# Optimization experiments

Measured on AMD Instinct MI355X. Metric: run time of the kernel, lower is better.

Reference implementation:

```python
import jax, jax.numpy as jnp
import numpy as np
import math

D_MODEL = 1024
H = 16
D_K = D_MODEL // H
D_FF = 4096
NEG = -1e9


def layer_norm(x, alpha, bias):
    # Faithful to source: mean over last dim, UNBIASED std (torch.std default),
    # eps defined in source but never used in forward.
    mean = jnp.mean(x, axis=-1, keepdims=True)
    std = jnp.std(x, axis=-1, ddof=1, keepdims=True)
    return (x - mean) / std * alpha + bias


def mha(x, mask, w_q, w_k, w_v, w_o):
    B, S, D = x.shape
    q = (x @ w_q.T).reshape(B, S, H, D_K)
    k = (x @ w_k.T).reshape(B, S, H, D_K)
    v = (x @ w_v.T).reshape(B, S, H, D_K)
    scores = jnp.einsum('bqhd,bkhd->bhqk', q, k) / math.sqrt(D_K)
    scores = jnp.where(mask, NEG, scores)
    attn = jax.nn.softmax(scores, axis=-1)
    out = jnp.einsum('bhqk,bkhd->bqhd', attn, v).reshape(B, S, D)
    return out @ w_o.T


def setup_inputs() -> dict:
    key = jax.random.key(0)
    ks = jax.random.split(key, 16)
    B, S = 4, 2048
    s = 0.02
    return {
        'x': jax.random.normal(ks[0], (B, S, D_MODEL), jnp.float32),
        'w_q': jax.random.normal(ks[1], (D_MODEL, D_MODEL), jnp.float32) * s,
        'w_k': jax.random.normal(ks[2], (D_MODEL, D_MODEL), jnp.float32) * s,
        'w_v': jax.random.normal(ks[3], (D_MODEL, D_MODEL), jnp.float32) * s,
        'w_o': jax.random.normal(ks[4], (D_MODEL, D_MODEL), jnp.float32) * s,
        'l1_w': jax.random.normal(ks[5], (D_FF, D_MODEL), jnp.float32) * s,
        'l1_b': jnp.zeros((D_FF,), jnp.float32),
        'l2_w': jax.random.normal(ks[6], (D_MODEL, D_FF), jnp.float32) * s,
        'l2_b': jnp.zeros((D_MODEL,), jnp.float32),
        'norm1_a': jnp.ones((D_MODEL,), jnp.float32),
        'norm1_b': jnp.zeros((D_MODEL,), jnp.float32),
        'norm2_a': jnp.ones((D_MODEL,), jnp.float32),
        'norm2_b': jnp.zeros((D_MODEL,), jnp.float32),
        'normf_a': jnp.ones((D_MODEL,), jnp.float32),
        'normf_b': jnp.zeros((D_MODEL,), jnp.float32),
        'mask': jax.random.randint(ks[7], (B, 1, 1, S), 0, 2) == 1,
    }


def reference(x, w_q, w_k, w_v, w_o, l1_w, l1_b, l2_w, l2_b,
              norm1_a, norm1_b, norm2_a, norm2_b, normf_a, normf_b, mask):
    # residual 1: pre-norm self-attention (dropout is identity at eval)
    x = x + mha(layer_norm(x, norm1_a, norm1_b), mask, w_q, w_k, w_v, w_o)
    # residual 2: pre-norm FFN
    h = layer_norm(x, norm2_a, norm2_b)
    ff = jax.nn.relu(h @ l1_w.T + l1_b) @ l2_w.T + l2_b
    x = x + ff
    return layer_norm(x, normf_a, normf_b)
```

## Files before the change

kernel.cpp:

```cpp
#include <hip/hip_runtime.h>
#include <hip/hip_bf16.h>


typedef __bf16 bf16x8 __attribute__((ext_vector_type(8)));
typedef float f32x4 __attribute__((ext_vector_type(4)));
typedef unsigned short u16x8 __attribute__((ext_vector_type(8)));
using bf16 = __hip_bfloat16;

__device__ __forceinline__ f32x4 mfma16(bf16x8 a, bf16x8 b, f32x4 c) {
  return __builtin_amdgcn_mfma_f32_16x16x32_bf16(a, b, c, 0, 0, 0);
}

__device__ __forceinline__ int swz(int row, int blk) {
  return row * 64 + ((blk ^ (row & 7)) << 3);
}

__device__ __forceinline__ void stage_tile64(unsigned short* lds,
                                             const bf16* g, int ld, int rows) {
  const int lane = threadIdx.x & 63, wid = threadIdx.x >> 6;
  const int r8 = lane >> 3, blk = lane & 7;
  const bf16* gl = g + (size_t)r8 * ld + ((blk ^ r8) << 3);
  const int passes = rows >> 3;
  for (int p = wid; p < passes; p += 4) {
    __builtin_amdgcn_global_load_lds(
        (const __attribute__((address_space(1))) void*)(gl + (size_t)(p * 8) * ld),
        (__attribute__((address_space(3))) void*)(lds + p * 512),
        16, 0, 0);
  }
}

__device__ __forceinline__ short bfb(float x) {
  return (short)__hip_bfloat16_raw(__float2bfloat16(x)).x;
}

__global__ __launch_bounds__(256) void cvt_k(const float* __restrict__ s,
                                             bf16* __restrict__ d, int n) {
  const int i = (blockIdx.x * 256 + threadIdx.x) * 4;
  if (i + 3 < n) {
    const float4 v = *reinterpret_cast<const float4*>(s + i);
    ushort4 o;
    o.x = (unsigned short)bfb(v.x);
    o.y = (unsigned short)bfb(v.y);
    o.z = (unsigned short)bfb(v.z);
    o.w = (unsigned short)bfb(v.w);
    *reinterpret_cast<ushort4*>(d + i) = o;
  }
}

template <bool OUT_F32>
__global__ __launch_bounds__(256) void layernorm_k(const float* __restrict__ in,
                                                   const float* __restrict__ gamma,
                                                   const float* __restrict__ beta,
                                                   void* __restrict__ out) {
  __shared__ float red[8];
  const int row = blockIdx.x, t = threadIdx.x;
  const float4 vv = reinterpret_cast<const float4*>(in + (size_t)row * 1024)[t];
  const float x0 = vv.x, x1 = vv.y, x2 = vv.z, x3 = vv.w;
  float s = x0 + x1 + x2 + x3;
#pragma unroll
  for (int off = 32; off; off >>= 1) s += __shfl_down(s, off);
  if ((t & 63) == 0) red[t >> 6] = s;
  __syncthreads();
  const float mean = (red[0] + red[1] + red[2] + red[3]) * (1.0f / 1024.0f);
  const float d0 = x0 - mean, d1 = x1 - mean, d2 = x2 - mean, d3 = x3 - mean;
  float sq = d0 * d0 + d1 * d1 + d2 * d2 + d3 * d3;
#pragma unroll
  for (int off = 32; off; off >>= 1) sq += __shfl_down(sq, off);
  if ((t & 63) == 0) red[4 + (t >> 6)] = sq;
  __syncthreads();
  const float var =
      fmaxf((red[4] + red[5] + red[6] + red[7]) * (1.0f / 1023.0f), 1e-20f);
  const float rstd = rsqrtf(var);
  const float4 ga = reinterpret_cast<const float4*>(gamma)[t];
  const float4 be = reinterpret_cast<const float4*>(beta)[t];
  const float y0 = d0 * rstd * ga.x + be.x;
  const float y1 = d1 * rstd * ga.y + be.y;
  const float y2 = d2 * rstd * ga.z + be.z;
  const float y3 = d3 * rstd * ga.w + be.w;
  if (OUT_F32) {
    reinterpret_cast<float4*>((float*)out + (size_t)row * 1024)[t] =
        make_float4(y0, y1, y2, y3);
  } else {
    ushort4 o;
    o.x = (unsigned short)bfb(y0);
    o.y = (unsigned short)bfb(y1);
    o.z = (unsigned short)bfb(y2);
    o.w = (unsigned short)bfb(y3);
    reinterpret_cast<ushort4*>((bf16*)out + (size_t)row * 1024)[t] = o;
  }
}

template <bool HAS_BIAS, bool RELU, bool HAS_RES, bool OUT_F32>
__global__ __launch_bounds__(256) void gemm_bt(const bf16* __restrict__ A,
                                               const bf16* __restrict__ W,
                                               const float* __restrict__ bias,
                                               const float* __restrict__ resid,
                                               void* __restrict__ out,
                                               int M, int N, int K,
                                               int lda, int ldw) {
  __shared__ __align__(16) unsigned short As[128 * 64];
  __shared__ __align__(16) unsigned short Bs[128 * 64];
  const int lane = threadIdx.x & 63, wid = threadIdx.x >> 6;
  const int n16 = lane & 15, quad = lane >> 4;
  const int wm = (wid >> 1) * 64, wn = (wid & 1) * 64;
  const int tm = blockIdx.x * 128, tn = blockIdx.y * 128;
  f32x4 acc[4][4] = {};
  for (int k0 = 0; k0 < K; k0 += 64) {
    stage_tile64(As, A + (size_t)tm * lda + k0, lda, 128);
    stage_tile64(Bs, W + (size_t)tn * ldw + k0, ldw, 128);
    __syncthreads();
#pragma unroll
    for (int kk = 0; kk < 64; kk += 32) {
      bf16x8 af[4], bw[4];
#pragma unroll
      for (int i = 0; i < 4; ++i)
        af[i] = *reinterpret_cast<const bf16x8*>(
            &As[swz(wm + i * 16 + n16, (kk >> 3) + quad)]);
#pragma unroll
      for (int j = 0; j < 4; ++j)
        bw[j] = *reinterpret_cast<const bf16x8*>(
            &Bs[swz(wn + j * 16 + n16, (kk >> 3) + quad)]);
#pragma unroll
      for (int i = 0; i < 4; ++i)
#pragma unroll
        for (int j = 0; j < 4; ++j) acc[i][j] = mfma16(af[i], bw[j], acc[i][j]);
    }
    __syncthreads();
  }
#pragma unroll
  for (int i = 0; i < 4; ++i) {
#pragma unroll
    for (int j = 0; j < 4; ++j) {
      const int n = tn + wn + j * 16 + n16;
      const float bv = HAS_BIAS ? bias[n] : 0.0f;
#pragma unroll
      for (int r = 0; r < 4; ++r) {
        const int m = tm + wm + i * 16 + quad * 4 + r;
        float vv = acc[i][j][r] + bv;
        if (RELU) vv = fmaxf(vv, 0.0f);
        if (HAS_RES) vv += resid[(size_t)m * N + n];
        if (OUT_F32)
          ((float*)out)[(size_t)m * N + n] = vv;
        else
          ((bf16*)out)[(size_t)m * N + n] = __float2bfloat16(vv);
      }
    }
  }
}

__global__ __launch_bounds__(256) void prep_mask_k(const int* __restrict__ m,
                                                   float* __restrict__ mf,
                                                   int n) {
  __shared__ int s;
  if (threadIdx.x == 0) s = 0;
  __syncthreads();
  unsigned int acc = 0;
  for (int i = threadIdx.x; i < 512; i += 256)
    acc |= ((const unsigned int*)m)[i] & 0xFFFFFF00u;
  if (acc) atomicOr(&s, 1);
  __syncthreads();
  const bool bytes = (s != 0);
  const int i = blockIdx.x * 256 + threadIdx.x;
  if (i < n) {
    const int v = bytes ? (int)((const unsigned char*)m)[i] : m[i];
    mf[i] = v ? -1.4427e9f : 0.0f;
  }
}

__global__ __launch_bounds__(256) void attn_k(const bf16* __restrict__ qkv,
                                              const float* __restrict__ maskf,
                                              bf16* __restrict__ out, int BHN) {
  __shared__ __align__(16) unsigned short Ks[2][64 * 64];
  __shared__ __align__(16) unsigned short Vs[2][64 * 72];
  const int lane = threadIdx.x & 63, wid = threadIdx.x >> 6;
  const int n16 = lane & 15, quad = lane >> 4;
  const int bid = blockIdx.x;
  const int bh = bid % BHN, qb = bid / BHN;
  const int b = bh >> 4, h = bh & 15;
  const size_t rowb = (size_t)b * 2048 * 3072;
  const bf16* qp0 = qkv + rowb + h * 64;
  const bf16* kp0 = qkv + rowb + 1024 + h * 64;
  const bf16* vp0 = qkv + rowb + 2048 + h * 64;
  const float* mfb = maskf + b * 2048;
  const int qrow0 = qb * 128 + wid * 32;

  bf16x8 qf[2][2];
#pragma unroll
  for (int g = 0; g < 2; ++g) {
    const bf16* qp = qp0 + (size_t)(qrow0 + g * 16 + n16) * 3072 + quad * 8;
    qf[g][0] = *reinterpret_cast<const bf16x8*>(qp);
    qf[g][1] = *reinterpret_cast<const bf16x8*>(qp + 32);
  }
  bf16x8 ones;
#pragma unroll
  for (int e = 0; e < 8; ++e) ones[e] = (__bf16)1.0f;
  f32x4 oacc[2][4] = {};
  f32x4 lacc[2] = {};
  const int prow = ((n16 >> 2) << 3) + (n16 & 3);
  const int vkey = lane, vdc = wid * 16;

  stage_tile64(Ks[0], kp0, 3072, 64);
  {
    const bf16* vp = vp0 + (size_t)vkey * 3072 + vdc;
    const u16x8 a = *reinterpret_cast<const u16x8*>(vp);
    const u16x8 bq = *reinterpret_cast<const u16x8*>(vp + 8);
#pragma unroll
    for (int e = 0; e < 8; ++e) {
      Vs[0][(vdc + e) * 72 + vkey] = a[e];
      Vs[0][(vdc + 8 + e) * 72 + vkey] = bq[e];
    }
  }
  int cur = 0;
  for (int kt = 0; kt < 2048; kt += 64) {
    __syncthreads();
    const bool hasNext = (kt + 64 < 2048);
    u16x8 na = {}, nb = {};
    if (hasNext) {
      stage_tile64(Ks[cur ^ 1], kp0 + (size_t)(kt + 64) * 3072, 3072, 64);
      const bf16* vp = vp0 + (size_t)(kt + 64 + vkey) * 3072 + vdc;
      na = *reinterpret_cast<const u16x8*>(vp);
      nb = *reinterpret_cast<const u16x8*>(vp + 8);
    }
    const unsigned short* Kc = Ks[cur];
    const unsigned short* Vc = Vs[cur];
#pragma unroll
    for (int sub = 0; sub < 2; ++sub) {
      const int kb = sub * 32;
      bf16x8 aflo[2], afhi[2];
#pragma unroll
      for (int st = 0; st < 2; ++st) {
        const int row = kb + prow + st * 4;
        aflo[st] = *reinterpret_cast<const bf16x8*>(&Kc[swz(row, quad)]);
        afhi[st] = *reinterpret_cast<const bf16x8*>(&Kc[swz(row, 4 + quad)]);
      }
      f32x4 z[2][2];
#pragma unroll
      for (int g = 0; g < 2; ++g)
#pragma unroll
        for (int st = 0; st < 2; ++st) {
          f32x4 zz = {};
          zz = mfma16(aflo[st], qf[g][0], zz);
          zz = mfma16(afhi[st], qf[g][1], zz);
          z[g][st] = zz;
        }
      const float4 m0 =
          *reinterpret_cast<const float4*>(mfb + kt + kb + quad * 8);
      const float4 m1 =
          *reinterpret_cast<const float4*>(mfb + kt + kb + quad * 8 + 4);
      bf16x8 vf[4];
#pragma unroll
      for (int j = 0; j < 4; ++j)
        vf[j] = *reinterpret_cast<const bf16x8*>(
            &Vc[(j * 16 + n16) * 72 + kb + quad * 8]);
#pragma unroll
      for (int g = 0; g < 2; ++g) {
        bf16x8 pf;
#pragma unroll
        for (int r = 0; r < 4; ++r) {
          const float e0 = __builtin_amdgcn_exp2f(
              fmaf(z[g][0][r], 0.18033688f, ((const float*)&m0)[r]));
          const float e1 = __builtin_amdgcn_exp2f(
              fmaf(z[g][1][r], 0.18033688f, ((const float*)&m1)[r]));
          pf[r] = (__bf16)e0;
          pf[4 + r] = (__bf16)e1;
        }
#pragma unroll
        for (int j = 0; j < 4; ++j) oacc[g][j] = mfma16(pf, vf[j], oacc[g][j]);
        lacc[g] = mfma16(pf, ones, lacc[g]);
      }
    }
    if (hasNext) {
      unsigned short* Vn = Vs[cur ^ 1];
#pragma unroll
      for (int e = 0; e < 8; ++e) {
        Vn[(vdc + e) * 72 + vkey] = na[e];
        Vn[(vdc + 8 + e) * 72 + vkey] = nb[e];
      }
    }
    cur ^= 1;
  }
#pragma unroll
  for (int g = 0; g < 2; ++g) {
#pragma unroll
    for (int r = 0; r < 4; ++r) {
      const float lr = 1.0f / fmaxf(lacc[g][r], 1e-20f);
      bf16* op =
          out + (size_t)(b * 2048 + qrow0 + g * 16 + quad * 4 + r) * 1024 +
          h * 64;
#pragma unroll
      for (int j = 0; j < 4; ++j)
        op[j * 16 + n16] = __float2bfloat16(oacc[g][j][r] * lr);
    }
  }
}

extern "C" void kernel_launch(void* const* d_in, const int* in_sizes, int n_in,
                              void* d_out, int out_size, void* d_ws,
                              size_t ws_size, hipStream_t stream) {
  const float* x    = (const float*)d_in[0];
  const float* w_q  = (const float*)d_in[1];
  const float* w_k  = (const float*)d_in[2];
  const float* w_v  = (const float*)d_in[3];
  const float* w_o  = (const float*)d_in[4];
  const float* l1_w = (const float*)d_in[5];
  const float* l1_b = (const float*)d_in[6];
  const float* l2_w = (const float*)d_in[7];
  const float* l2_b = (const float*)d_in[8];
  const float* n1a  = (const float*)d_in[9];
  const float* n1b  = (const float*)d_in[10];
  const float* n2a  = (const float*)d_in[11];
  const float* n2b  = (const float*)d_in[12];
  const float* nfa  = (const float*)d_in[13];
  const float* nfb  = (const float*)d_in[14];
  const int* mask   = (const int*)d_in[15];

  const int D = 1024, FF = 4096;
  const int M = in_sizes[0] / D;

  const size_t MB = 1024ull * 1024ull;
  if (ws_size < 121 * MB) return;
  char* w = (char*)d_ws;
  bf16* WQKV = (bf16*)(w + 0 * MB);
  bf16* WO   = (bf16*)(w + 6 * MB);
  bf16* L1W  = (bf16*)(w + 8 * MB);
  bf16* L2W  = (bf16*)(w + 16 * MB);
  bf16* LN1  = (bf16*)(w + 24 * MB);
  bf16* QKV  = (bf16*)(w + 40 * MB);
  bf16* ATT  = LN1;
  bf16* HLN  = (bf16*)(w + 40 * MB);
  bf16* FF1  = (bf16*)(w + 56 * MB);
  float* X1  = (float*)(w + 88 * MB);
  float* MASKF = (float*)(w + 120 * MB);

  const dim3 blk(256);
  cvt_k<<<dim3(D * D / 1024), blk, 0, stream>>>(w_q, WQKV, D * D);
  cvt_k<<<dim3(D * D / 1024), blk, 0, stream>>>(w_k, WQKV + D * D, D * D);
  cvt_k<<<dim3(D * D / 1024), blk, 0, stream>>>(w_v, WQKV + 2 * D * D, D * D);
  cvt_k<<<dim3(D * D / 1024), blk, 0, stream>>>(w_o, WO, D * D);
  cvt_k<<<dim3(FF * D / 1024), blk, 0, stream>>>(l1_w, L1W, FF * D);
  cvt_k<<<dim3(FF * D / 1024), blk, 0, stream>>>(l2_w, L2W, FF * D);
  prep_mask_k<<<dim3((M + 255) / 256), blk, 0, stream>>>(mask, MASKF, M);

  layernorm_k<false><<<M, blk, 0, stream>>>(x, n1a, n1b, LN1);
  gemm_bt<false, false, false, false>
      <<<dim3(M / 128, 3072 / 128), blk, 0, stream>>>(LN1, WQKV, nullptr,
                                                      nullptr, QKV, M, 3072, D,
                                                      D, D);
  const int BHN = (M / 2048) * 16;
  attn_k<<<dim3((M / 128) * 16), blk, 0, stream>>>(QKV, MASKF, ATT, BHN);
  gemm_bt<false, false, true, true><<<dim3(M / 128, D / 128), blk, 0, stream>>>(
      ATT, WO, nullptr, x, X1, M, D, D, D, D);
  layernorm_k<false><<<M, blk, 0, stream>>>(X1, n2a, n2b, HLN);
  for (int c = 0; c < 2; ++c) {
    gemm_bt<true, true, false, false>
        <<<dim3(M / 128, 2048 / 128), blk, 0, stream>>>(
            HLN, L1W + (size_t)c * 2048 * D, l1_b + c * 2048, nullptr, FF1, M,
            2048, D, D, D);
    if (c == 0)
      gemm_bt<true, false, true, true>
          <<<dim3(M / 128, D / 128), blk, 0, stream>>>(
              FF1, L2W + c * 2048, l2_b, X1, X1, M, D, 2048, 2048, FF);
    else
      gemm_bt<false, false, true, true>
          <<<dim3(M / 128, D / 128), blk, 0, stream>>>(
              FF1, L2W + c * 2048, nullptr, X1, X1, M, D, 2048, 2048, FF);
  }
  layernorm_k<true><<<M, blk, 0, stream>>>(X1, nfa, nfb, (float*)d_out);
}
```

Baseline: 574.7 us.

## Compact unmasked keys and values so attention skips masked key tiles

Adds a per-batch prefix-scan kernel that builds an index list of unmasked key positions plus a compacted mask, and a gather kernel that copies those K/V rows, zero-padded to a multiple of 64, into a dense buffer. The attention kernel then loops only over the padded count of valid keys instead of all 2048, cutting QK and PV MFMA work and K/V traffic roughly in proportion to the masked fraction. In exchange it adds two extra launches and a full K/V copy through a workspace region it shares with X1. It also raises wave priority around the MFMA blocks with s_setprio.

```diff
diff --git a/kernel.cpp b/kernel.cpp
--- a/kernel.cpp
+++ b/kernel.cpp
@@ -167,8 +167,65 @@
   }
 }
 
+__global__ __launch_bounds__(256) void scan_k(const float* __restrict__ maskf,
+                                              float* __restrict__ cmask,
+                                              int* __restrict__ idx,
+                                              int* __restrict__ cnt) {
+  __shared__ int wsum[4];
+  const int b = blockIdx.x, t = threadIdx.x, lane = t & 63, w = t >> 6;
+  const float* mrow = maskf + b * 2048;
+  int keep[8], local = 0;
+#pragma unroll
+  for (int e = 0; e < 8; ++e) {
+    keep[e] = (mrow[t * 8 + e] == 0.0f) ? 1 : 0;
+    local += keep[e];
+  }
+  int inc = local;
+#pragma unroll
+  for (int off = 1; off < 64; off <<= 1) {
+    int v = __shfl_up(inc, off);
+    if (lane >= off) inc += v;
+  }
+  if (lane == 63) wsum[w] = inc;
+  __syncthreads();
+  int base = 0;
+#pragma unroll
+  for (int i = 0; i < 4; ++i)
+    if (i < w) base += wsum[i];
+  int p = base + inc - local;
+#pragma unroll
+  for (int e = 0; e < 8; ++e)
+    if (keep[e]) idx[b * 2048 + p++] = t * 8 + e;
+  const int total = wsum[0] + wsum[1] + wsum[2] + wsum[3];
+  if (t == 0) cnt[b] = total;
+  for (int i = t; i < 2048; i += 256)
+    cmask[b * 2048 + i] = (i < total) ? 0.0f : -1.4427e9f;
+}
+
+__global__ __launch_bounds__(256) void gather_k(const bf16* __restrict__ qkv,
+                                                const int* __restrict__ idx,
+                                                const int* __restrict__ cnt,
+                                                bf16* __restrict__ kv) {
+  const int b = blockIdx.x >> 11, j = blockIdx.x & 2047;
+  const int n = cnt[b];
+  const int npad = (n + 63) & ~63;
+  if (j >= npad) return;
+  u16x8* dst = reinterpret_cast<u16x8*>(kv + ((size_t)(b * 2048 + j)) * 2048);
+  if (j < n) {
+    const int s = idx[b * 2048 + j];
+    const u16x8* src = reinterpret_cast<const u16x8*>(
+        qkv + ((size_t)(b * 2048 + s)) * 3072 + 1024);
+    dst[threadIdx.x] = src[threadIdx.x];
+  } else {
+    u16x8 z = {};
+    dst[threadIdx.x] = z;
+  }
+}
+
 __global__ __launch_bounds__(256) void attn_k(const bf16* __restrict__ qkv,
-                                              const float* __restrict__ maskf,
+                                              const bf16* __restrict__ kv,
+                                              const float* __restrict__ cmask,
+                                              const int* __restrict__ cnt,
                                               bf16* __restrict__ out, int BHN) {
   __shared__ __align__(16) unsigned short Ks[2][64 * 64];
   __shared__ __align__(16) unsigned short Vs[2][64 * 72];
@@ -179,9 +236,10 @@
   const int b = bh >> 4, h = bh & 15;
   const size_t rowb = (size_t)b * 2048 * 3072;
   const bf16* qp0 = qkv + rowb + h * 64;
-  const bf16* kp0 = qkv + rowb + 1024 + h * 64;
-  const bf16* vp0 = qkv + rowb + 2048 + h * 64;
-  const float* mfb = maskf + b * 2048;
+  const bf16* kp0 = kv + (size_t)b * 2048 * 2048 + h * 64;
+  const bf16* vp0 = kp0 + 1024;
+  const float* mfb = cmask + b * 2048;
+  const int nk = ((cnt[b] + 63) >> 6) << 6;
   const int qrow0 = qb * 128 + wid * 32;
 
   bf16x8 qf[2][2];
@@ -199,9 +257,9 @@
   const int prow = ((n16 >> 2) << 3) + (n16 & 3);
   const int vkey = lane, vdc = wid * 16;
 
-  stage_tile64(Ks[0], kp0, 3072, 64);
+  stage_tile64(Ks[0], kp0, 2048, 64);
   {
-    const bf16* vp = vp0 + (size_t)vkey * 3072 + vdc;
+    const bf16* vp = vp0 + (size_t)vkey * 2048 + vdc;
     const u16x8 a = *reinterpret_cast<const u16x8*>(vp);
     const u16x8 bq = *reinterpret_cast<const u16x8*>(vp + 8);
 #pragma unroll
@@ -211,13 +269,13 @@
     }
   }
   int cur = 0;
-  for (int kt = 0; kt < 2048; kt += 64) {
+  for (int kt = 0; kt < nk; kt += 64) {
     __syncthreads();
-    const bool hasNext = (kt + 64 < 2048);
+    const bool hasNext = (kt + 64 < nk);
     u16x8 na = {}, nb = {};
     if (hasNext) {
-      stage_tile64(Ks[cur ^ 1], kp0 + (size_t)(kt + 64) * 3072, 3072, 64);
-      const bf16* vp = vp0 + (size_t)(kt + 64 + vkey) * 3072 + vdc;
+      stage_tile64(Ks[cur ^ 1], kp0 + (size_t)(kt + 64) * 2048, 2048, 64);
+      const bf16* vp = vp0 + (size_t)(kt + 64 + vkey) * 2048 + vdc;
       na = *reinterpret_cast<const u16x8*>(vp);
       nb = *reinterpret_cast<const u16x8*>(vp + 8);
     }
@@ -233,6 +291,7 @@
         aflo[st] = *reinterpret_cast<const bf16x8*>(&Kc[swz(row, quad)]);
         afhi[st] = *reinterpret_cast<const bf16x8*>(&Kc[swz(row, 4 + quad)]);
       }
+      __builtin_amdgcn_s_setprio(1);
       f32x4 z[2][2];
 #pragma unroll
       for (int g = 0; g < 2; ++g)
@@ -243,6 +302,7 @@
           zz = mfma16(afhi[st], qf[g][1], zz);
           z[g][st] = zz;
         }
+      __builtin_amdgcn_s_setprio(0);
       const float4 m0 =
           *reinterpret_cast<const float4*>(mfb + kt + kb + quad * 8);
       const float4 m1 =
@@ -264,9 +324,11 @@
           pf[r] = (__bf16)e0;
           pf[4 + r] = (__bf16)e1;
         }
+        __builtin_amdgcn_s_setprio(1);
 #pragma unroll
         for (int j = 0; j < 4; ++j) oacc[g][j] = mfma16(pf, vf[j], oacc[g][j]);
         lacc[g] = mfma16(pf, ones, lacc[g]);
+        __builtin_amdgcn_s_setprio(0);
       }
     }
     if (hasNext) {
@@ -316,6 +378,7 @@
 
   const int D = 1024, FF = 4096;
   const int M = in_sizes[0] / D;
+  const int B = M / 2048;
 
   const size_t MB = 1024ull * 1024ull;
   if (ws_size < 121 * MB) return;
@@ -329,8 +392,12 @@
   bf16* ATT  = LN1;
   bf16* HLN  = (bf16*)(w + 40 * MB);
   bf16* FF1  = (bf16*)(w + 56 * MB);
+  bf16* KV   = (bf16*)(w + 88 * MB);
   float* X1  = (float*)(w + 88 * MB);
   float* MASKF = (float*)(w + 120 * MB);
+  float* CMASK = (float*)(w + 120 * MB + 256 * 1024);
+  int*   IDX   = (int*)(w + 120 * MB + 512 * 1024);
+  int*   CNT   = (int*)(w + 120 * MB + 768 * 1024);
 
   const dim3 blk(256);
   cvt_k<<<dim3(D * D / 1024), blk, 0, stream>>>(w_q, WQKV, D * D);
@@ -340,14 +407,17 @@
   cvt_k<<<dim3(FF * D / 1024), blk, 0, stream>>>(l1_w, L1W, FF * D);
   cvt_k<<<dim3(FF * D / 1024), blk, 0, stream>>>(l2_w, L2W, FF * D);
   prep_mask_k<<<dim3((M + 255) / 256), blk, 0, stream>>>(mask, MASKF, M);
+  scan_k<<<dim3(B), blk, 0, stream>>>(MASKF, CMASK, IDX, CNT);
 
   layernorm_k<false><<<M, blk, 0, stream>>>(x, n1a, n1b, LN1);
   gemm_bt<false, false, false, false>
       <<<dim3(M / 128, 3072 / 128), blk, 0, stream>>>(LN1, WQKV, nullptr,
                                                       nullptr, QKV, M, 3072, D,
                                                       D, D);
-  const int BHN = (M / 2048) * 16;
-  attn_k<<<dim3((M / 128) * 16), blk, 0, stream>>>(QKV, MASKF, ATT, BHN);
+  gather_k<<<dim3(B * 2048), blk, 0, stream>>>(QKV, IDX, CNT, KV);
+  const int BHN = B * 16;
+  attn_k<<<dim3((M / 128) * 16), blk, 0, stream>>>(QKV, KV, CMASK, CNT, ATT,
+                                                   BHN);
   gemm_bt<false, false, true, true><<<dim3(M / 128, D / 128), blk, 0, stream>>>(
       ATT, WO, nullptr, x, X1, M, D, D, D, D);
   layernorm_k<false><<<M, blk, 0, stream>>>(X1, n2a, n2b, HLN);
```

New measurement: 520.1 us. 1.1x faster.
